# Kernel tuning notes

Hardware: AMD Instinct MI355X
Metric: run time of the kernel (lower is better)

## Reference

```python
import jax, jax.numpy as jnp
import numpy as np

N = 100000
E = 3200000
IN_DIM = 128
OUT_DIM = 128
BN_EPS = 1e-5
LEAKY_SLOPE = 0.01


def setup_inputs() -> dict:
    key = jax.random.key(0)
    ks = jax.random.split(key, 6)
    fea = jax.random.normal(ks[0], (N, IN_DIM), dtype=jnp.float32)
    edges = jax.random.randint(ks[1], (2, E), 0, N, dtype=jnp.int64)
    Wlin = jax.random.normal(ks[2], (IN_DIM, IN_DIM), dtype=jnp.float32) * (1.0 / np.sqrt(IN_DIM))
    blin = jax.random.normal(ks[3], (IN_DIM,), dtype=jnp.float32) * 0.01
    gamma = jnp.ones((IN_DIM,), dtype=jnp.float32)
    beta = jnp.zeros((IN_DIM,), dtype=jnp.float32)
    Wg = jax.random.normal(ks[4], (OUT_DIM, IN_DIM), dtype=jnp.float32) * (1.0 / np.sqrt(IN_DIM))
    bg = jnp.zeros((OUT_DIM,), dtype=jnp.float32)
    return {"fea": fea, "edges": edges, "Wlin": Wlin, "blin": blin,
            "gamma": gamma, "beta": beta, "Wg": Wg, "bg": bg}


def reference(fea, edges, Wlin, blin, gamma, beta, Wg, bg):
    n = fea.shape[0]
    # Linear (in_dim -> in_dim)
    x = fea @ Wlin.T + blin
    # BatchNorm1d, training-mode batch statistics over the node dimension
    mean = jnp.mean(x, axis=0)
    var = jnp.var(x, axis=0)
    x = gamma * (x - mean) * jax.lax.rsqrt(var + BN_EPS) + beta
    # Dropout(p=0.0) is identity; LeakyReLU
    x = jnp.where(x >= 0, x, LEAKY_SLOPE * x)
    # GCNConv: h = x W^T, then D^-1/2 (A+I) D^-1/2 aggregation + bias
    h = x @ Wg.T  # [N, out_dim]
    self_idx = jnp.arange(n, dtype=edges.dtype)
    src = jnp.concatenate([edges[0], self_idx])
    dst = jnp.concatenate([edges[1], self_idx])
    deg = jax.ops.segment_sum(jnp.ones_like(dst, dtype=h.dtype), dst, num_segments=n)
    dinv = jnp.where(deg > 0, jax.lax.rsqrt(deg), 0.0)
    norm = dinv[src] * dinv[dst]  # [E+N]
    msgs = norm[:, None] * h[src]  # [E+N, out_dim]
    out = jax.ops.segment_sum(msgs, dst, num_segments=n) + bg
    # LogSoftmax over feature dim
    return jax.nn.log_softmax(out, axis=1)
```

## Files before the change

kernel.cpp:

```cpp
#include <hip/hip_runtime.h>
#include <math.h>

#define LEAKY 0.01f
#define BN_EPS 1e-5f
#define NBLK 512
#define EBUF 10240

typedef unsigned int uint;
typedef float f32x2 __attribute__((ext_vector_type(2)));
typedef float f32x4 __attribute__((ext_vector_type(4)));
typedef short bf16x8 __attribute__((ext_vector_type(8)));

__device__ __forceinline__ float bflo(uint v) { return __uint_as_float(v << 16); }
__device__ __forceinline__ float bfhi(uint v) { return __uint_as_float(v & 0xffff0000u); }
__device__ __forceinline__ uint packbf(float a, float b) {
    uint ua = __float_as_uint(a), ub = __float_as_uint(b);
    ua += 0x7fffu + ((ua >> 16) & 1u);
    ub += 0x7fffu + ((ub >> 16) & 1u);
    return (ua >> 16) | (ub & 0xffff0000u);
}

__device__ __forceinline__ int detect_i64(const int* __restrict__ raw) {
    int t = threadIdx.x & 63;
    unsigned long long b = __ballot(raw[2 * t + 1] != 0);
    return b == 0ull;
}

__device__ __forceinline__ void build_bbase(const int* __restrict__ btot,
                                            int NBUK, int* bb, int* sd)
{
    const int t = threadIdx.x;
    int a0 = (2 * t     < NBUK) ? btot[2 * t]     : 0;
    int a1 = (2 * t + 1 < NBUK) ? btot[2 * t + 1] : 0;
    int s = a0 + a1;
    sd[t] = s;
    __syncthreads();
    for (int o = 1; o < 256; o <<= 1) {
        int u = (t >= o) ? sd[t - o] : 0;
        __syncthreads();
        sd[t] += u;
        __syncthreads();
    }
    int ex = sd[t] - s;
    bb[2 * t]     = ex;
    bb[2 * t + 1] = ex + a0;
    __syncthreads();
}

__global__ __launch_bounds__(256) void k_prep(const float* __restrict__ Wlin,
                                              const float* __restrict__ Wg,
                                              uint* __restrict__ Wlinb,
                                              uint* __restrict__ Wgb,
                                              float* __restrict__ sumsr)
{
    const int idx = blockIdx.x * 256 + threadIdx.x;
    if (blockIdx.x < 32) sumsr[blockIdx.x * 256 + threadIdx.x] = 0.f;
    if (idx < 8192) {
        Wlinb[idx] = packbf(Wlin[2 * idx], Wlin[2 * idx + 1]);
    } else {
        int j = idx - 8192;
        Wgb[j] = packbf(Wg[2 * j], Wg[2 * j + 1]);
    }
}

__global__ __launch_bounds__(256) void k_front(const float* __restrict__ fea,
                                               const uint* __restrict__ Wb,
                                               const float* __restrict__ bias,
                                               uint* __restrict__ xb,
                                               float* __restrict__ sumsr,
                                               const void* __restrict__ edges, int E,
                                               int* __restrict__ histm,
                                               int NBUK, int N, int G_lin)
{
    __shared__ uint smem[4352];
    const int tid = threadIdx.x;

    if ((int)blockIdx.x >= G_lin) {
        const int bid = blockIdx.x - G_lin;
        int* hh = (int*)smem;
        for (int b = tid; b < 512; b += 256) hh[b] = 0;
        const int isI64 = detect_i64((const int*)edges);
        __syncthreads();
        const long long* e64 = (const long long*)edges;
        const int*       e32 = (const int*)edges;
        const int chunk = (E + NBLK - 1) / NBLK;
        const int lo = bid * chunk;
        const int hi = min(lo + chunk, E);
        for (int e = lo + tid; e < hi; e += 256) {
            int dst = isI64 ? (int)e64[(size_t)E + e] : e32[(size_t)E + e];
            atomicAdd(&hh[dst >> 8], 1);
        }
        __syncthreads();
        for (int b = tid; b < NBUK; b += 256)
            histm[(size_t)b * NBLK + bid] = hh[b];
        return;
    }

    const int r0   = blockIdx.x * 64;
    const int lane = tid & 63;
    const int w    = tid >> 6;
    const int fr   = lane & 15;
    const int fk   = lane >> 4;

    #pragma unroll
    for (int it = 0; it < 8; ++it) {
        int flat = it * 256 + tid;
        int row  = flat >> 5;
        int c4   = flat & 31;
        int r    = r0 + row;
        float4 v = make_float4(0.f, 0.f, 0.f, 0.f);
        if (r < N) v = *reinterpret_cast<const float4*>(&fea[(size_t)r * 128 + c4 * 4]);
        smem[row * 68 + c4 * 2]     = packbf(v.x, v.y);
        smem[row * 68 + c4 * 2 + 1] = packbf(v.z, v.w);
    }
    __syncthreads();

    bf16x8 a[4];
    #pragma unroll
    for (int kk = 0; kk < 4; ++kk)
        a[kk] = *reinterpret_cast<const bf16x8*>(
            &smem[(w * 16 + fr) * 68 + kk * 16 + fk * 4]);

    f32x4 acc[8] = {};
    #pragma unroll
    for (int jt = 0; jt < 8; ++jt) {
        #pragma unroll
        for (int kk = 0; kk < 4; ++kk) {
            bf16x8 b = *reinterpret_cast<const bf16x8*>(
                &Wb[(size_t)(jt * 16 + fr) * 64 + kk * 16 + fk * 4]);
            acc[jt] = __builtin_amdgcn_mfma_f32_16x16x32_bf16(a[kk], b, acc[jt], 0, 0, 0);
        }
    }
    __syncthreads();

    float* sred = (float*)smem;
    float* qred = sred + 2048;
    #pragma unroll
    for (int jt = 0; jt < 8; ++jt) {
        float bj = bias[jt * 16 + fr];
        float sl = 0.f, ql = 0.f;
        #pragma unroll
        for (int r = 0; r < 4; ++r) {
            int gr = r0 + w * 16 + fk * 4 + r;
            float val = acc[jt][r] + bj;
            val = (gr < N) ? val : 0.f;
            acc[jt][r] = val;
            sl += val; ql += val * val;
        }
        sred[(w * 4 + fk) * 128 + jt * 16 + fr] = sl;
        qred[(w * 4 + fk) * 128 + jt * 16 + fr] = ql;
    }
    __syncthreads();
    if (tid < 128) {
        float S = 0.f, Q = 0.f;
        #pragma unroll
        for (int g = 0; g < 16; ++g) {
            S += sred[g * 128 + tid];
            Q += qred[g * 128 + tid];
        }
        float* dstp = sumsr + (blockIdx.x & 31) * 256;
        atomicAdd(&dstp[tid], S);
        atomicAdd(&dstp[128 + tid], Q);
    }
    __syncthreads();

    #pragma unroll
    for (int jt = 0; jt < 8; ++jt) {
        #pragma unroll
        for (int r = 0; r < 4; ++r) {
            float val = acc[jt][r];
            float pv  = __shfl_xor(val, 1);
            if ((lane & 1) == 0)
                smem[(w * 16 + fk * 4 + r) * 68 + jt * 8 + (fr >> 1)] = packbf(val, pv);
        }
    }
    __syncthreads();
    #pragma unroll
    for (int it = 0; it < 4; ++it) {
        int idx4 = it * 256 + tid;
        int row  = idx4 >> 4;
        int c4   = idx4 & 15;
        if (r0 + row < N) {
            uint4 v = *reinterpret_cast<const uint4*>(&smem[row * 68 + c4 * 4]);
            *reinterpret_cast<uint4*>(&xb[(size_t)(r0 + row) * 64 + c4 * 4]) = v;
        }
    }
}

__global__ __launch_bounds__(512) void k_bscan(int* __restrict__ histm,
                                               int* __restrict__ btot)
{
    __shared__ int sd[512];
    const int bkt = blockIdx.x;
    const int t = threadIdx.x;
    int v = histm[(size_t)bkt * NBLK + t];
    sd[t] = v;
    __syncthreads();
    for (int o = 1; o < 512; o <<= 1) {
        int u = (t >= o) ? sd[t - o] : 0;
        __syncthreads();
        sd[t] += u;
        __syncthreads();
    }
    histm[(size_t)bkt * NBLK + t] = sd[t] - v;
    if (t == 511) btot[bkt] = sd[511];
}

__global__ __launch_bounds__(256) void k_binscatter(const void* __restrict__ edges, int E,
                                                    const int* __restrict__ histm,
                                                    const int* __restrict__ btot,
                                                    uint* __restrict__ bins, int NBUK)
{
    __shared__ int cur[512];
    __shared__ int bb[512];
    __shared__ int sd[256];
    const int isI64 = detect_i64((const int*)edges);
    build_bbase(btot, NBUK, bb, sd);
    for (int b = threadIdx.x; b < NBUK; b += 256)
        cur[b] = bb[b] + histm[(size_t)b * NBLK + blockIdx.x];
    __syncthreads();

    const long long* e64 = (const long long*)edges;
    const int*       e32 = (const int*)edges;
    const int chunk = (E + NBLK - 1) / NBLK;
    const int lo = blockIdx.x * chunk;
    const int hi = min(lo + chunk, E);
    for (int e = lo + threadIdx.x; e < hi; e += 256) {
        int src, dst;
        if (isI64) { src = (int)e64[e]; dst = (int)e64[(size_t)E + e]; }
        else       { src = e32[e];      dst = e32[(size_t)E + e]; }
        int pos = atomicAdd(&cur[dst >> 8], 1);
        bins[pos] = (uint)src | ((uint)(dst & 255) << 24);
    }
}

__global__ __launch_bounds__(256) void k_csrdeg(const uint* __restrict__ bins,
                                                const int* __restrict__ btot,
                                                int* __restrict__ pcnt,
                                                float* __restrict__ dinv,
                                                int* __restrict__ offs,
                                                uint* __restrict__ csr,
                                                int N, int NBUK)
{
    __shared__ uint ebuf[EBUF];
    __shared__ int bb[512];
    __shared__ int sd[256];
    __shared__ int c[256];
    const int bkt = blockIdx.x;
    const int t = threadIdx.x;
    build_bbase(btot, NBUK, bb, sd);
    const int lo    = bb[bkt];
    const int total = btot[bkt];
    c[t] = 0;
    __syncthreads();

    const bool fits = (total <= EBUF);
    for (int i = t; i < total; i += 256) {
        uint e = bins[lo + i];
        if (fits) ebuf[i] = e;
        atomicAdd(&c[e >> 24], 1);
    }
    __syncthreads();

    const int node = (bkt << 8) + t;
    const int deg  = c[t];
    const int pdeg = (deg + 15) & ~15;
    if (node < N) {
        pcnt[node] = pdeg;
        dinv[node] = rsqrtf((float)(deg + 1));
    }
    sd[t] = pdeg;
    __syncthreads();
    for (int o = 1; o < 256; o <<= 1) {
        int u = (t >= o) ? sd[t - o] : 0;
        __syncthreads();
        sd[t] += u;
        __syncthreads();
    }
    const int myoff = lo + (bkt << 12) + sd[t] - pdeg;
    if (node < N) offs[node] = myoff;
    c[t] = myoff;
    __syncthreads();
    for (int i = t; i < total; i += 256) {
        uint e = fits ? ebuf[i] : bins[lo + i];
        int pos = atomicAdd(&c[e >> 24], 1);
        csr[pos] = e & 0x00ffffffu;
    }
    for (int k2 = deg; k2 < pdeg; ++k2)
        csr[myoff + k2] = (uint)N;
}

__global__ __launch_bounds__(256) void k_h(const uint* __restrict__ xb,
                                           const uint* __restrict__ Wb,
                                           const float* __restrict__ sumsr,
                                           const float* __restrict__ gamma,
                                           const float* __restrict__ beta,
                                           const float* __restrict__ dinv,
                                           float invN,
                                           uint* __restrict__ hb, int N)
{
    __shared__ uint xls[4352];
    __shared__ float aff[256];
    const int tid  = threadIdx.x;
    const int r0   = blockIdx.x * 64;
    const int lane = tid & 63;
    const int w    = tid >> 6;
    const int fr   = lane & 15;
    const int fk   = lane >> 4;

    if (tid < 128) {
        float S = 0.f, Q = 0.f;
        #pragma unroll
        for (int rep = 0; rep < 32; ++rep) {
            S += sumsr[rep * 256 + tid];
            Q += sumsr[rep * 256 + 128 + tid];
        }
        float mean = S * invN;
        float var  = Q * invN - mean * mean;
        float coef = gamma[tid] * rsqrtf(var + BN_EPS);
        aff[tid]       = coef;
        aff[128 + tid] = beta[tid] - coef * mean;
    }
    __syncthreads();

    #pragma unroll
    for (int it = 0; it < 16; ++it) {
        int flat = it * 256 + tid;
        int row  = flat >> 6;
        int u    = flat & 63;
        int r    = r0 + row;
        uint v   = (r < N) ? xb[(size_t)r * 64 + u] : 0u;
        float y0 = fmaf(aff[2 * u],     bflo(v), aff[128 + 2 * u]);
        float y1 = fmaf(aff[2 * u + 1], bfhi(v), aff[128 + 2 * u + 1]);
        y0 = (y0 >= 0.f) ? y0 : LEAKY * y0;
        y1 = (y1 >= 0.f) ? y1 : LEAKY * y1;
        xls[row * 68 + u] = packbf(y0, y1);
    }
    __syncthreads();

    bf16x8 a[4];
    #pragma unroll
    for (int kk = 0; kk < 4; ++kk)
        a[kk] = *reinterpret_cast<const bf16x8*>(
            &xls[(w * 16 + fr) * 68 + kk * 16 + fk * 4]);

    f32x4 acc[8] = {};
    #pragma unroll
    for (int jt = 0; jt < 8; ++jt) {
        #pragma unroll
        for (int kk = 0; kk < 4; ++kk) {
            bf16x8 b = *reinterpret_cast<const bf16x8*>(
                &Wb[(size_t)(jt * 16 + fr) * 64 + kk * 16 + fk * 4]);
            acc[jt] = __builtin_amdgcn_mfma_f32_16x16x32_bf16(a[kk], b, acc[jt], 0, 0, 0);
        }
    }

    float dv[4];
    #pragma unroll
    for (int r = 0; r < 4; ++r) {
        int gr = r0 + w * 16 + fk * 4 + r;
        dv[r] = (gr < N) ? dinv[gr] : 0.f;
    }
    __syncthreads();

    #pragma unroll
    for (int jt = 0; jt < 8; ++jt) {
        #pragma unroll
        for (int r = 0; r < 4; ++r) {
            float val = acc[jt][r] * dv[r];
            float p1  = __shfl_xor(val, 1);
            uint lo16 = (uint)__builtin_amdgcn_cvt_pk_fp8_f32(val, p1, 0, false) & 0xffffu;
            uint hi16 = __shfl_xor(lo16, 2);
            if ((fr & 3) == 0)
                xls[(w * 16 + fk * 4 + r) * 36 + jt * 4 + (fr >> 2)] = lo16 | (hi16 << 16);
        }
    }
    __syncthreads();
    #pragma unroll
    for (int it = 0; it < 2; ++it) {
        int idx4 = it * 256 + tid;
        int row  = idx4 >> 3;
        int c4   = idx4 & 7;
        if (r0 + row <= N) {
            uint4 v = *reinterpret_cast<const uint4*>(&xls[row * 36 + c4 * 4]);
            *reinterpret_cast<uint4*>(&hb[(size_t)(r0 + row) * 32 + c4 * 4]) = v;
        }
    }
}

__global__ __launch_bounds__(256) void k_agg(const uint* __restrict__ hb,
                                             const uint* __restrict__ csr,
                                             const int* __restrict__ offs,
                                             const int* __restrict__ pcnt,
                                             const float* __restrict__ dinv,
                                             const float* __restrict__ bg,
                                             float* __restrict__ out, int N)
{
    const int wid  = (blockIdx.x * blockDim.x + threadIdx.x) >> 6;
    const int lane = threadIdx.x & 63;
    if (wid >= N) return;
    const int i = wid;
    const int p = lane & 15;
    const int q = lane >> 4;
    const uint2* hbp = reinterpret_cast<const uint2*>(hb) + p;

    f32x2 acc[4] = {};
    const int start = offs[i];
    const int m     = pcnt[i];

    for (int base = 0; base < m; base += 64) {
        const int nb = min(64, m - base);
        uint sx = (uint)N;
        if (lane < nb)
            sx = __builtin_nontemporal_load(&csr[start + base + lane]);
        for (int j = 0; j < nb; j += 16) {
            int s0 = __shfl((int)sx, j + q);
            int s1 = __shfl((int)sx, j + 4 + q);
            int s2 = __shfl((int)sx, j + 8 + q);
            int s3 = __shfl((int)sx, j + 12 + q);
            const uint2 v0 = hbp[(uint)s0 * 16];
            const uint2 v1 = hbp[(uint)s1 * 16];
            const uint2 v2 = hbp[(uint)s2 * 16];
            const uint2 v3 = hbp[(uint)s3 * 16];
            acc[0] += __builtin_amdgcn_cvt_pk_f32_fp8((int)v0.x, false);
            acc[1] += __builtin_amdgcn_cvt_pk_f32_fp8((int)v0.x, true);
            acc[2] += __builtin_amdgcn_cvt_pk_f32_fp8((int)v0.y, false);
            acc[3] += __builtin_amdgcn_cvt_pk_f32_fp8((int)v0.y, true);
            acc[0] += __builtin_amdgcn_cvt_pk_f32_fp8((int)v1.x, false);
            acc[1] += __builtin_amdgcn_cvt_pk_f32_fp8((int)v1.x, true);
            acc[2] += __builtin_amdgcn_cvt_pk_f32_fp8((int)v1.y, false);
            acc[3] += __builtin_amdgcn_cvt_pk_f32_fp8((int)v1.y, true);
            acc[0] += __builtin_amdgcn_cvt_pk_f32_fp8((int)v2.x, false);
            acc[1] += __builtin_amdgcn_cvt_pk_f32_fp8((int)v2.x, true);
            acc[2] += __builtin_amdgcn_cvt_pk_f32_fp8((int)v2.y, false);
            acc[3] += __builtin_amdgcn_cvt_pk_f32_fp8((int)v2.y, true);
            acc[0] += __builtin_amdgcn_cvt_pk_f32_fp8((int)v3.x, false);
            acc[1] += __builtin_amdgcn_cvt_pk_f32_fp8((int)v3.x, true);
            acc[2] += __builtin_amdgcn_cvt_pk_f32_fp8((int)v3.y, false);
            acc[3] += __builtin_amdgcn_cvt_pk_f32_fp8((int)v3.y, true);
        }
    }

    #pragma unroll
    for (int r = 0; r < 4; ++r) {
        acc[r].x += __shfl_xor(acc[r].x, 16);
        acc[r].y += __shfl_xor(acc[r].y, 16);
        acc[r].x += __shfl_xor(acc[r].x, 32);
        acc[r].y += __shfl_xor(acc[r].y, 32);
    }

    const uint2 sv = hbp[(uint)i * 16];
    acc[0] += __builtin_amdgcn_cvt_pk_f32_fp8((int)sv.x, false);
    acc[1] += __builtin_amdgcn_cvt_pk_f32_fp8((int)sv.x, true);
    acc[2] += __builtin_amdgcn_cvt_pk_f32_fp8((int)sv.y, false);
    acc[3] += __builtin_amdgcn_cvt_pk_f32_fp8((int)sv.y, true);

    const float d0 = dinv[i];
    float4 b0 = *reinterpret_cast<const float4*>(&bg[p * 8]);
    float4 b1 = *reinterpret_cast<const float4*>(&bg[p * 8 + 4]);
    float v0 = fmaf(d0, acc[0].x, b0.x);
    float v1 = fmaf(d0, acc[0].y, b0.y);
    float v2 = fmaf(d0, acc[1].x, b0.z);
    float v3 = fmaf(d0, acc[1].y, b0.w);
    float v4 = fmaf(d0, acc[2].x, b1.x);
    float v5 = fmaf(d0, acc[2].y, b1.y);
    float v6 = fmaf(d0, acc[3].x, b1.z);
    float v7 = fmaf(d0, acc[3].y, b1.w);

    float mx = fmaxf(fmaxf(fmaxf(v0, v1), fmaxf(v2, v3)),
                     fmaxf(fmaxf(v4, v5), fmaxf(v6, v7)));
    #pragma unroll
    for (int o = 8; o > 0; o >>= 1) mx = fmaxf(mx, __shfl_xor(mx, o));
    float sum = __expf(v0 - mx) + __expf(v1 - mx) + __expf(v2 - mx) + __expf(v3 - mx)
              + __expf(v4 - mx) + __expf(v5 - mx) + __expf(v6 - mx) + __expf(v7 - mx);
    #pragma unroll
    for (int o = 8; o > 0; o >>= 1) sum += __shfl_xor(sum, o);
    float ls = mx + __logf(sum);

    if (q == 0) {
        f32x4 o0 = {v0 - ls, v1 - ls, v2 - ls, v3 - ls};
        f32x4 o1 = {v4 - ls, v5 - ls, v6 - ls, v7 - ls};
        __builtin_nontemporal_store(o0, reinterpret_cast<f32x4*>(&out[(size_t)i * 128 + p * 8]));
        __builtin_nontemporal_store(o1, reinterpret_cast<f32x4*>(&out[(size_t)i * 128 + p * 8 + 4]));
    }
}

extern "C" void kernel_launch(void* const* d_in, const int* in_sizes, int n_in,
                              void* d_out, int out_size, void* d_ws, size_t ws_size,
                              hipStream_t stream)
{
    (void)n_in; (void)out_size; (void)ws_size;
    const float* fea   = (const float*)d_in[0];
    const void*  edges = d_in[1];
    const float* Wlin  = (const float*)d_in[2];
    const float* blin  = (const float*)d_in[3];
    const float* gamma = (const float*)d_in[4];
    const float* beta  = (const float*)d_in[5];
    const float* Wg    = (const float*)d_in[6];
    const float* bg    = (const float*)d_in[7];
    float* out = (float*)d_out;

    const int N    = in_sizes[0] / 128;
    const int E    = in_sizes[1] / 2;
    const int NBUK = (N + 255) >> 8;
    const int GLIN = (N + 63) / 64;

    char* p = (char*)d_ws;
    uint*  xb   = (uint*)p;    p += (size_t)N * 64 * 4;
    uint*  bins = (uint*)p;    p += (size_t)E * 4;
    uint*  hb   = (uint*)p;    p += ((size_t)N + 1) * 32 * 4;
    uint*  csr  = (uint*)p;    p += ((size_t)E + ((size_t)NBUK << 12)) * 4;
    int*   histm = (int*)p;    p += (size_t)NBUK * NBLK * 4;
    float* sumsr = (float*)p;  p += 32 * 256 * 4;
    int*   pcnt = (int*)p;     p += (size_t)N * 4;
    int*   offs = (int*)p;     p += (size_t)N * 4;
    float* dinv = (float*)p;   p += (size_t)N * 4;
    int*   btot = (int*)p;     p += 512 * 4;
    uint*  Wlinb = (uint*)p;   p += 8192 * 4;
    uint*  Wgb   = (uint*)p;   p += 8192 * 4;

    k_prep<<<64, 256, 0, stream>>>(Wlin, Wg, Wlinb, Wgb, sumsr);

    k_front<<<GLIN + NBLK, 256, 0, stream>>>(fea, Wlinb, blin, xb, sumsr,
                                             edges, E, histm, NBUK, N, GLIN);

    k_bscan<<<NBUK, 512, 0, stream>>>(histm, btot);
    k_binscatter<<<NBLK, 256, 0, stream>>>(edges, E, histm, btot, bins, NBUK);
    k_csrdeg<<<NBUK, 256, 0, stream>>>(bins, btot, pcnt, dinv, offs, csr, N, NBUK);

    k_h<<<(N + 64) / 64, 256, 0, stream>>>(xb, Wgb, sumsr, gamma, beta, dinv,
                                           1.0f / (float)N, hb, N);

    k_agg<<<(N + 3) / 4, 256, 0, stream>>>(hb, csr, offs, pcnt, dinv, bg, out, N);
}
```

Before: 222.4 us.

## Fuse preprocessing kernels into one cooperative persistent kernel with grid syncs

Merges the weight-packing, linear+BN stats, bucket histogram, bucket scan, bin scatter, CSR/degree build and h-projection stages into a single cooperative kernel of 512 blocks separated by grid-wide syncs. The goal is to remove the launch gaps and tail idle time between six small kernels. In exchange, each block now loops over many linear/h tiles at low occupancy, since 44 KB of shared memory is used per block. If the cooperative launch fails, it falls back to the separate kernels.

```diff
diff --git a/kernel.cpp b/kernel.cpp
--- a/kernel.cpp
+++ b/kernel.cpp
@@ -1,10 +1,14 @@
 #include <hip/hip_runtime.h>
+#include <hip/hip_cooperative_groups.h>
 #include <math.h>
+
+namespace cg = cooperative_groups;
 
 #define LEAKY 0.01f
 #define BN_EPS 1e-5f
 #define NBLK 512
 #define EBUF 10240
+#define GRID 512
 
 typedef unsigned int uint;
 typedef float f32x2 __attribute__((ext_vector_type(2)));
@@ -47,56 +51,16 @@
     __syncthreads();
 }
 
-__global__ __launch_bounds__(256) void k_prep(const float* __restrict__ Wlin,
-                                              const float* __restrict__ Wg,
-                                              uint* __restrict__ Wlinb,
-                                              uint* __restrict__ Wgb,
-                                              float* __restrict__ sumsr)
-{
-    const int idx = blockIdx.x * 256 + threadIdx.x;
-    if (blockIdx.x < 32) sumsr[blockIdx.x * 256 + threadIdx.x] = 0.f;
-    if (idx < 8192) {
-        Wlinb[idx] = packbf(Wlin[2 * idx], Wlin[2 * idx + 1]);
-    } else {
-        int j = idx - 8192;
-        Wgb[j] = packbf(Wg[2 * j], Wg[2 * j + 1]);
-    }
-}
-
-__global__ __launch_bounds__(256) void k_front(const float* __restrict__ fea,
-                                               const uint* __restrict__ Wb,
-                                               const float* __restrict__ bias,
-                                               uint* __restrict__ xb,
-                                               float* __restrict__ sumsr,
-                                               const void* __restrict__ edges, int E,
-                                               int* __restrict__ histm,
-                                               int NBUK, int N, int G_lin)
-{
-    __shared__ uint smem[4352];
-    const int tid = threadIdx.x;
-
-    if ((int)blockIdx.x >= G_lin) {
-        const int bid = blockIdx.x - G_lin;
-        int* hh = (int*)smem;
-        for (int b = tid; b < 512; b += 256) hh[b] = 0;
-        const int isI64 = detect_i64((const int*)edges);
-        __syncthreads();
-        const long long* e64 = (const long long*)edges;
-        const int*       e32 = (const int*)edges;
-        const int chunk = (E + NBLK - 1) / NBLK;
-        const int lo = bid * chunk;
-        const int hi = min(lo + chunk, E);
-        for (int e = lo + tid; e < hi; e += 256) {
-            int dst = isI64 ? (int)e64[(size_t)E + e] : e32[(size_t)E + e];
-            atomicAdd(&hh[dst >> 8], 1);
-        }
-        __syncthreads();
-        for (int b = tid; b < NBUK; b += 256)
-            histm[(size_t)b * NBLK + bid] = hh[b];
-        return;
-    }
-
-    const int r0   = blockIdx.x * 64;
+
+__device__ __forceinline__ void lin_tile_body(uint* smem, int tile, int repsel,
+                                              const float* __restrict__ fea,
+                                              const uint* __restrict__ Wb,
+                                              const float* __restrict__ bias,
+                                              uint* __restrict__ xb,
+                                              float* __restrict__ sumsr, int N)
+{
+    const int tid  = threadIdx.x;
+    const int r0   = tile * 64;
     const int lane = tid & 63;
     const int w    = tid >> 6;
     const int fr   = lane & 15;
@@ -158,7 +122,7 @@
             S += sred[g * 128 + tid];
             Q += qred[g * 128 + tid];
         }
-        float* dstp = sumsr + (blockIdx.x & 31) * 256;
+        float* dstp = sumsr + (repsel & 31) * 256;
         atomicAdd(&dstp[tid], S);
         atomicAdd(&dstp[128 + tid], Q);
     }
@@ -185,45 +149,76 @@
             *reinterpret_cast<uint4*>(&xb[(size_t)(r0 + row) * 64 + c4 * 4]) = v;
         }
     }
-}
-
-__global__ __launch_bounds__(512) void k_bscan(int* __restrict__ histm,
-                                               int* __restrict__ btot)
-{
-    __shared__ int sd[512];
-    const int bkt = blockIdx.x;
+    __syncthreads();
+}
+
+__device__ __forceinline__ void bhist_body(uint* smem, int bid,
+                                           const void* __restrict__ edges, int E,
+                                           int* __restrict__ histm, int NBUK)
+{
+    const int tid = threadIdx.x;
+    int* hh = (int*)smem;
+    for (int b = tid; b < 512; b += 256) hh[b] = 0;
+    const int isI64 = detect_i64((const int*)edges);
+    __syncthreads();
+    const long long* e64 = (const long long*)edges;
+    const int*       e32 = (const int*)edges;
+    const int chunk = (E + NBLK - 1) / NBLK;
+    const int lo = bid * chunk;
+    const int hi = min(lo + chunk, E);
+    for (int e = lo + tid; e < hi; e += 256) {
+        int dst = isI64 ? (int)e64[(size_t)E + e] : e32[(size_t)E + e];
+        atomicAdd(&hh[dst >> 8], 1);
+    }
+    __syncthreads();
+    for (int b = tid; b < NBUK; b += 256)
+        histm[(size_t)b * NBLK + bid] = hh[b];
+    __syncthreads();
+}
+
+__device__ __forceinline__ void bscan_body(uint* smem, int bkt,
+                                           int* __restrict__ histm,
+                                           int* __restrict__ btot)
+{
     const int t = threadIdx.x;
-    int v = histm[(size_t)bkt * NBLK + t];
-    sd[t] = v;
-    __syncthreads();
-    for (int o = 1; o < 512; o <<= 1) {
+    int* sd = (int*)smem;
+    int a0 = histm[(size_t)bkt * NBLK + 2 * t];
+    int a1 = histm[(size_t)bkt * NBLK + 2 * t + 1];
+    int s = a0 + a1;
+    sd[t] = s;
+    __syncthreads();
+    for (int o = 1; o < 256; o <<= 1) {
         int u = (t >= o) ? sd[t - o] : 0;
         __syncthreads();
         sd[t] += u;
         __syncthreads();
     }
-    histm[(size_t)bkt * NBLK + t] = sd[t] - v;
-    if (t == 511) btot[bkt] = sd[511];
-}
-
-__global__ __launch_bounds__(256) void k_binscatter(const void* __restrict__ edges, int E,
-                                                    const int* __restrict__ histm,
-                                                    const int* __restrict__ btot,
-                                                    uint* __restrict__ bins, int NBUK)
-{
-    __shared__ int cur[512];
-    __shared__ int bb[512];
-    __shared__ int sd[256];
+    int ex = sd[t] - s;
+    histm[(size_t)bkt * NBLK + 2 * t]     = ex;
+    histm[(size_t)bkt * NBLK + 2 * t + 1] = ex + a0;
+    if (t == 255) btot[bkt] = ex + a0 + a1;
+    __syncthreads();
+}
+
+__device__ __forceinline__ void binscatter_body(uint* smem, int bid,
+                                                const void* __restrict__ edges, int E,
+                                                const int* __restrict__ histm,
+                                                const int* __restrict__ btot,
+                                                uint* __restrict__ bins, int NBUK)
+{
+    int* cur = (int*)smem;
+    int* bb  = (int*)smem + 512;
+    int* sd  = (int*)smem + 1024;
     const int isI64 = detect_i64((const int*)edges);
     build_bbase(btot, NBUK, bb, sd);
     for (int b = threadIdx.x; b < NBUK; b += 256)
-        cur[b] = bb[b] + histm[(size_t)b * NBLK + blockIdx.x];
+        cur[b] = bb[b] + histm[(size_t)b * NBLK + bid];
     __syncthreads();
 
     const long long* e64 = (const long long*)edges;
     const int*       e32 = (const int*)edges;
     const int chunk = (E + NBLK - 1) / NBLK;
-    const int lo = blockIdx.x * chunk;
+    const int lo = bid * chunk;
     const int hi = min(lo + chunk, E);
     for (int e = lo + threadIdx.x; e < hi; e += 256) {
         int src, dst;
@@ -232,21 +227,22 @@
         int pos = atomicAdd(&cur[dst >> 8], 1);
         bins[pos] = (uint)src | ((uint)(dst & 255) << 24);
     }
-}
-
-__global__ __launch_bounds__(256) void k_csrdeg(const uint* __restrict__ bins,
-                                                const int* __restrict__ btot,
-                                                int* __restrict__ pcnt,
-                                                float* __restrict__ dinv,
-                                                int* __restrict__ offs,
-                                                uint* __restrict__ csr,
-                                                int N, int NBUK)
-{
-    __shared__ uint ebuf[EBUF];
-    __shared__ int bb[512];
-    __shared__ int sd[256];
-    __shared__ int c[256];
-    const int bkt = blockIdx.x;
+    __syncthreads();
+}
+
+__device__ __forceinline__ void csrdeg_body(uint* smem, int bkt,
+                                            const uint* __restrict__ bins,
+                                            const int* __restrict__ btot,
+                                            int* __restrict__ pcnt,
+                                            float* __restrict__ dinv,
+                                            int* __restrict__ offs,
+                                            uint* __restrict__ csr,
+                                            int N, int NBUK)
+{
+    uint* ebuf = smem;
+    int* bb = (int*)(smem + 10240);
+    int* sd = (int*)(smem + 10752);
+    int* c  = (int*)(smem + 11008);
     const int t = threadIdx.x;
     build_bbase(btot, NBUK, bb, sd);
     const int lo    = bb[bkt];
@@ -288,26 +284,17 @@
     }
     for (int k2 = deg; k2 < pdeg; ++k2)
         csr[myoff + k2] = (uint)N;
-}
-
-__global__ __launch_bounds__(256) void k_h(const uint* __restrict__ xb,
-                                           const uint* __restrict__ Wb,
+    __syncthreads();
+}
+
+__device__ __forceinline__ void h_aff_body(uint* smem,
                                            const float* __restrict__ sumsr,
                                            const float* __restrict__ gamma,
                                            const float* __restrict__ beta,
-                                           const float* __restrict__ dinv,
-                                           float invN,
-                                           uint* __restrict__ hb, int N)
-{
-    __shared__ uint xls[4352];
-    __shared__ float aff[256];
-    const int tid  = threadIdx.x;
-    const int r0   = blockIdx.x * 64;
-    const int lane = tid & 63;
-    const int w    = tid >> 6;
-    const int fr   = lane & 15;
-    const int fk   = lane >> 4;
-
+                                           float invN)
+{
+    float* aff = (float*)(smem + 4352);
+    const int tid = threadIdx.x;
     if (tid < 128) {
         float S = 0.f, Q = 0.f;
         #pragma unroll
@@ -322,6 +309,22 @@
         aff[128 + tid] = beta[tid] - coef * mean;
     }
     __syncthreads();
+}
+
+__device__ __forceinline__ void h_tile_body(uint* smem, int tile,
+                                            const uint* __restrict__ xb,
+                                            const uint* __restrict__ Wb,
+                                            const float* __restrict__ dinv,
+                                            uint* __restrict__ hb, int N)
+{
+    uint* xls = smem;
+    float* aff = (float*)(smem + 4352);
+    const int tid  = threadIdx.x;
+    const int r0   = tile * 64;
+    const int lane = tid & 63;
+    const int w    = tid >> 6;
+    const int fr   = lane & 15;
+    const int fk   = lane >> 4;
 
     #pragma unroll
     for (int it = 0; it < 16; ++it) {
@@ -386,6 +389,134 @@
             *reinterpret_cast<uint4*>(&hb[(size_t)(r0 + row) * 32 + c4 * 4]) = v;
         }
     }
+    __syncthreads();
+}
+
+__global__ __launch_bounds__(256) void k_mega(
+    const float* __restrict__ fea, const void* __restrict__ edges,
+    const float* __restrict__ Wlin, const float* __restrict__ blin,
+    const float* __restrict__ gamma, const float* __restrict__ beta,
+    const float* __restrict__ Wg,
+    uint* __restrict__ xb, uint* __restrict__ bins, uint* __restrict__ hb,
+    uint* __restrict__ csr, int* __restrict__ histm, float* __restrict__ sumsr,
+    int* __restrict__ pcnt, int* __restrict__ offs, float* __restrict__ dinv,
+    int* __restrict__ btot, uint* __restrict__ Wlinb, uint* __restrict__ Wgb,
+    int E, int N, int NBUK, int GLIN, int GH, float invN)
+{
+    cg::grid_group g = cg::this_grid();
+    __shared__ __align__(16) uint smem[11264];
+    const int tid = threadIdx.x;
+    const int bid = blockIdx.x;
+
+    {
+        int idx = bid * 256 + tid;
+        if (idx < 8192) {
+            Wlinb[idx] = packbf(Wlin[2 * idx], Wlin[2 * idx + 1]);
+        } else if (idx < 16384) {
+            int j = idx - 8192;
+            Wgb[j] = packbf(Wg[2 * j], Wg[2 * j + 1]);
+        }
+        if (bid < 32) sumsr[bid * 256 + tid] = 0.f;
+    }
+    __threadfence();
+    g.sync();
+
+    for (int tile = bid; tile < GLIN; tile += GRID)
+        lin_tile_body(smem, tile, bid, fea, Wlinb, blin, xb, sumsr, N);
+    bhist_body(smem, bid, edges, E, histm, NBUK);
+    __threadfence();
+    g.sync();
+
+    if (bid < NBUK) bscan_body(smem, bid, histm, btot);
+    __threadfence();
+    g.sync();
+
+    binscatter_body(smem, bid, edges, E, histm, btot, bins, NBUK);
+    __threadfence();
+    g.sync();
+
+    if (bid < NBUK) csrdeg_body(smem, bid, bins, btot, pcnt, dinv, offs, csr, N, NBUK);
+    __threadfence();
+    g.sync();
+
+    h_aff_body(smem, sumsr, gamma, beta, invN);
+    for (int tile = bid; tile < GH; tile += GRID)
+        h_tile_body(smem, tile, xb, Wgb, dinv, hb, N);
+}
+
+__global__ __launch_bounds__(256) void k_prep(const float* __restrict__ Wlin,
+                                              const float* __restrict__ Wg,
+                                              uint* __restrict__ Wlinb,
+                                              uint* __restrict__ Wgb,
+                                              float* __restrict__ sumsr)
+{
+    const int idx = blockIdx.x * 256 + threadIdx.x;
+    if (blockIdx.x < 32) sumsr[blockIdx.x * 256 + threadIdx.x] = 0.f;
+    if (idx < 8192) {
+        Wlinb[idx] = packbf(Wlin[2 * idx], Wlin[2 * idx + 1]);
+    } else {
+        int j = idx - 8192;
+        Wgb[j] = packbf(Wg[2 * j], Wg[2 * j + 1]);
+    }
+}
+
+__global__ __launch_bounds__(256) void k_front(const float* __restrict__ fea,
+                                               const uint* __restrict__ Wb,
+                                               const float* __restrict__ bias,
+                                               uint* __restrict__ xb,
+                                               float* __restrict__ sumsr,
+                                               const void* __restrict__ edges, int E,
+                                               int* __restrict__ histm,
+                                               int NBUK, int N, int G_lin)
+{
+    __shared__ __align__(16) uint smem[4352];
+    if ((int)blockIdx.x >= G_lin) {
+        bhist_body(smem, blockIdx.x - G_lin, edges, E, histm, NBUK);
+        return;
+    }
+    lin_tile_body(smem, blockIdx.x, blockIdx.x, fea, Wb, bias, xb, sumsr, N);
+}
+
+__global__ __launch_bounds__(256) void k_bscan2(int* __restrict__ histm,
+                                                int* __restrict__ btot)
+{
+    __shared__ uint smem[256];
+    bscan_body(smem, blockIdx.x, histm, btot);
+}
+
+__global__ __launch_bounds__(256) void k_binscatter(const void* __restrict__ edges, int E,
+                                                    const int* __restrict__ histm,
+                                                    const int* __restrict__ btot,
+                                                    uint* __restrict__ bins, int NBUK)
+{
+    __shared__ uint smem[1280];
+    binscatter_body(smem, blockIdx.x, edges, E, histm, btot, bins, NBUK);
+}
+
+__global__ __launch_bounds__(256) void k_csrdeg(const uint* __restrict__ bins,
+                                                const int* __restrict__ btot,
+                                                int* __restrict__ pcnt,
+                                                float* __restrict__ dinv,
+                                                int* __restrict__ offs,
+                                                uint* __restrict__ csr,
+                                                int N, int NBUK)
+{
+    __shared__ __align__(16) uint smem[11264];
+    csrdeg_body(smem, blockIdx.x, bins, btot, pcnt, dinv, offs, csr, N, NBUK);
+}
+
+__global__ __launch_bounds__(256) void k_h(const uint* __restrict__ xb,
+                                           const uint* __restrict__ Wb,
+                                           const float* __restrict__ sumsr,
+                                           const float* __restrict__ gamma,
+                                           const float* __restrict__ beta,
+                                           const float* __restrict__ dinv,
+                                           float invN,
+                                           uint* __restrict__ hb, int N)
+{
+    __shared__ __align__(16) uint smem[4608];
+    h_aff_body(smem, sumsr, gamma, beta, invN);
+    h_tile_body(smem, blockIdx.x, xb, Wb, dinv, hb, N);
 }
 
 __global__ __launch_bounds__(256) void k_agg(const uint* __restrict__ hb,
@@ -504,6 +635,8 @@
     const int E    = in_sizes[1] / 2;
     const int NBUK = (N + 255) >> 8;
     const int GLIN = (N + 63) / 64;
+    const int GH   = (N + 64) / 64;
+    const float invN = 1.0f / (float)N;
 
     char* p = (char*)d_ws;
     uint*  xb   = (uint*)p;    p += (size_t)N * 64 * 4;
@@ -519,17 +652,27 @@
     uint*  Wlinb = (uint*)p;   p += 8192 * 4;
     uint*  Wgb   = (uint*)p;   p += 8192 * 4;
 
-    k_prep<<<64, 256, 0, stream>>>(Wlin, Wg, Wlinb, Wgb, sumsr);
-
-    k_front<<<GLIN + NBLK, 256, 0, stream>>>(fea, Wlinb, blin, xb, sumsr,
-                                             edges, E, histm, NBUK, N, GLIN);
-
-    k_bscan<<<NBUK, 512, 0, stream>>>(histm, btot);
-    k_binscatter<<<NBLK, 256, 0, stream>>>(edges, E, histm, btot, bins, NBUK);
-    k_csrdeg<<<NBUK, 256, 0, stream>>>(bins, btot, pcnt, dinv, offs, csr, N, NBUK);
-
-    k_h<<<(N + 64) / 64, 256, 0, stream>>>(xb, Wgb, sumsr, gamma, beta, dinv,
-                                           1.0f / (float)N, hb, N);
+    int e_ = E, n_ = N, nbuk_ = NBUK, glin_ = GLIN, gh_ = GH;
+    float invn_ = invN;
+    void* kargs[] = { (void*)&fea, (void*)&edges, (void*)&Wlin, (void*)&blin,
+                      (void*)&gamma, (void*)&beta, (void*)&Wg,
+                      (void*)&xb, (void*)&bins, (void*)&hb, (void*)&csr,
+                      (void*)&histm, (void*)&sumsr, (void*)&pcnt, (void*)&offs,
+                      (void*)&dinv, (void*)&btot, (void*)&Wlinb, (void*)&Wgb,
+                      (void*)&e_, (void*)&n_, (void*)&nbuk_, (void*)&glin_,
+                      (void*)&gh_, (void*)&invn_ };
+    hipError_t cerr = hipLaunchCooperativeKernel((const void*)k_mega,
+                                                 dim3(GRID), dim3(256),
+                                                 kargs, 0, stream);
+    if (cerr != hipSuccess) {
+        k_prep<<<64, 256, 0, stream>>>(Wlin, Wg, Wlinb, Wgb, sumsr);
+        k_front<<<GLIN + NBLK, 256, 0, stream>>>(fea, Wlinb, blin, xb, sumsr,
+                                                 edges, E, histm, NBUK, N, GLIN);
+        k_bscan2<<<NBUK, 256, 0, stream>>>(histm, btot);
+        k_binscatter<<<NBLK, 256, 0, stream>>>(edges, E, histm, btot, bins, NBUK);
+        k_csrdeg<<<NBUK, 256, 0, stream>>>(bins, btot, pcnt, dinv, offs, csr, N, NBUK);
+        k_h<<<GH, 256, 0, stream>>>(xb, Wgb, sumsr, gamma, beta, dinv, invN, hb, N);
+    }
 
     k_agg<<<(N + 3) / 4, 256, 0, stream>>>(hb, csr, offs, pcnt, dinv, bg, out, N);
 }
```

Result: slower. 801.7 us (+260.5%).
